# Kernel tuning notes

Hardware: AMD Instinct MI355X
Metric: run time of the kernel (lower is better)

## Reference

```python
import jax, jax.numpy as jnp
import numpy as np

WINDOW_SIZE = 11
SIGMA = 1.5
C1 = 0.01 ** 2
C2 = 0.03 ** 2


def _gaussian_window(window_size, sigma, channel):
    xs = np.arange(window_size)
    g = np.exp(-((xs - window_size // 2) ** 2) / (2.0 * sigma ** 2))
    g = (g / g.sum()).astype(np.float32)
    w2d = np.outer(g, g)  # [k,k]
    # depthwise kernel layout OIHW with O=channel, I=1
    return jnp.asarray(np.broadcast_to(w2d, (channel, 1, window_size, window_size)).copy())


def _blur(x, window, channel):
    # depthwise conv, SAME-style padding = k//2 (k odd -> exact SAME)
    pad = WINDOW_SIZE // 2
    return jax.lax.conv_general_dilated(
        x, window,
        window_strides=(1, 1),
        padding=[(pad, pad), (pad, pad)],
        dimension_numbers=('NCHW', 'OIHW', 'NCHW'),
        feature_group_count=channel,
    )


def setup_inputs() -> dict:
    key = jax.random.key(0)
    k1, k2 = jax.random.split(key)
    shape = (32, 3, 512, 512)
    img1 = jax.random.uniform(k1, shape, dtype=jnp.float32)
    img2 = jax.random.uniform(k2, shape, dtype=jnp.float32)
    return {"img1": img1, "img2": img2}


def reference(img1, img2):
    channel = img1.shape[1]
    window = _gaussian_window(WINDOW_SIZE, SIGMA, channel).astype(img1.dtype)

    mu1 = _blur(img1, window, channel)
    mu2 = _blur(img2, window, channel)
    mu1_sq = mu1 * mu1
    mu2_sq = mu2 * mu2
    mu1_mu2 = mu1 * mu2

    sigma1_sq = _blur(img1 * img1, window, channel) - mu1_sq
    sigma2_sq = _blur(img2 * img2, window, channel) - mu2_sq
    sigma12 = _blur(img1 * img2, window, channel) - mu1_mu2

    ssim_map = ((2 * mu1_mu2 + C1) * (2 * sigma12 + C2)) / (
        (mu1_sq + mu2_sq + C1) * (sigma1_sq + sigma2_sq + C2))
    return 1.0 - jnp.mean(ssim_map)
```

## Files before the change

### kernel.cpp

```cpp
#include <hip/hip_runtime.h>


#define HH 512
#define WW 512
#define TILE 32
#define IN_ROWS 42
#define S_STRIDE 50
#define H_STRIDE 32
#define NPLANES 96
#define NPIX 25165824.0f
#define NACC 256
#define NTASK 672

#define H0123_OFF 0
#define H4_OFF  21504
#define UNION_BYTES 26880

typedef float v2f __attribute__((ext_vector_type(2)));
typedef float v4f __attribute__((ext_vector_type(4)));

__global__ __launch_bounds__(256, 6) void ssim_fused_kernel(
    const float* __restrict__ img1, const float* __restrict__ img2,
    float* __restrict__ acc) {
  __shared__ __align__(16) char ub[UNION_BYTES];
  __shared__ float wsum[4];

  v2f (*s12)[S_STRIDE] = (v2f (*)[S_STRIDE])ub;
  v4f (*h0123)[H_STRIDE] = (v4f (*)[H_STRIDE])(ub + H0123_OFF);
  float (*h4)[H_STRIDE] = (float (*)[H_STRIDE])(ub + H4_OFF);

  const int tid = threadIdx.x;
  const int tx = blockIdx.x * TILE;
  const int ty = blockIdx.y * TILE;
  const size_t base = (size_t)blockIdx.z * (HH * WW);

  const float g[11] = {
      1.0283800e-03f, 7.5987600e-03f, 3.6000770e-02f, 1.0936072e-01f,
      2.1300560e-01f, 2.6601170e-01f, 2.1300560e-01f, 1.0936072e-01f,
      3.6000770e-02f, 7.5987600e-03f, 1.0283800e-03f};

#pragma unroll
  for (int it = 0; it < 2; ++it) {
    int idx = it * 256 + tid;
    if (idx < IN_ROWS * 12) {
      int r = idx / 12;
      int p = idx - r * 12;
      int gy = ty - 5 + r;
      int gx = tx - 8 + 4 * p;
      v4f A = {0.f, 0.f, 0.f, 0.f}, B = {0.f, 0.f, 0.f, 0.f};
      if ((unsigned)gy < (unsigned)HH && (unsigned)gx < (unsigned)WW) {
        size_t off = base + (size_t)gy * WW + gx;
        A = *(const v4f*)(img1 + off);
        B = *(const v4f*)(img2 + off);
      }
      *(v4f*)&s12[r][4 * p]     = (v4f){A.x, B.x, A.y, B.y};
      *(v4f*)&s12[r][4 * p + 2] = (v4f){A.z, B.z, A.w, B.w};
    }
  }
  __syncthreads();

  v2f hold01[3][2], hold23[3][2], hold4[3];
#pragma unroll
  for (int t = 0; t < 3; ++t) {
    int idx = t * 256 + tid;
    if (idx < NTASK) {
      int r = idx >> 4;
      int c = (idx & 15) * 2;
      const v4f* qp = (const v4f*)&s12[r][c + 2];
      v4f q0 = qp[0], q1 = qp[1], q2 = qp[2], q3 = qp[3];
      v4f q4 = qp[4], q5 = qp[5], q6 = qp[6];
      v2f P[14];
      P[0]  = (v2f){q0.x, q0.y};  P[1]  = (v2f){q0.z, q0.w};
      P[2]  = (v2f){q1.x, q1.y};  P[3]  = (v2f){q1.z, q1.w};
      P[4]  = (v2f){q2.x, q2.y};  P[5]  = (v2f){q2.z, q2.w};
      P[6]  = (v2f){q3.x, q3.y};  P[7]  = (v2f){q3.z, q3.w};
      P[8]  = (v2f){q4.x, q4.y};  P[9]  = (v2f){q4.z, q4.w};
      P[10] = (v2f){q5.x, q5.y};  P[11] = (v2f){q5.z, q5.w};
      P[12] = (v2f){q6.x, q6.y};  P[13] = (v2f){q6.z, q6.w};

      v2f a01_0 = (v2f){0.f, 0.f}, a23_0 = (v2f){0.f, 0.f};
      v2f a01_1 = (v2f){0.f, 0.f}, a23_1 = (v2f){0.f, 0.f};
      float a4_0 = 0.f, a4_1 = 0.f;
#pragma unroll
      for (int k = 1; k <= 12; ++k) {
        v2f p = P[k];
        v2f sq = p * p;
        float cr = p.x * p.y;
        if (k <= 11) {
          float w = g[k - 1];
          a01_0 += w * p;
          a23_0 += w * sq;
          a4_0 = __builtin_fmaf(w, cr, a4_0);
        }
        if (k >= 2) {
          float w = g[k - 2];
          a01_1 += w * p;
          a23_1 += w * sq;
          a4_1 = __builtin_fmaf(w, cr, a4_1);
        }
      }
      hold01[t][0] = a01_0;  hold01[t][1] = a01_1;
      hold23[t][0] = a23_0;  hold23[t][1] = a23_1;
      hold4[t] = (v2f){a4_0, a4_1};
    }
  }
  __syncthreads();

#pragma unroll
  for (int t = 0; t < 3; ++t) {
    int idx = t * 256 + tid;
    if (idx < NTASK) {
      int r = idx >> 4;
      int c = (idx & 15) * 2;
      *(v4f*)&h0123[r][c]     = (v4f){hold01[t][0].x, hold01[t][0].y,
                                      hold23[t][0].x, hold23[t][0].y};
      *(v4f*)&h0123[r][c + 1] = (v4f){hold01[t][1].x, hold01[t][1].y,
                                      hold23[t][1].x, hold23[t][1].y};
      *(v2f*)&h4[r][c] = hold4[t];
    }
  }
  __syncthreads();

  const float C1 = 1e-4f;
  const float C2 = 9e-4f;
  const int c = tid & 31;
  const int r0 = (tid >> 5) * 4;

  v2f m[4], vv[4];
  float b12[4];
#pragma unroll
  for (int o = 0; o < 4; ++o) {
    m[o] = (v2f){0.f, 0.f};
    vv[o] = (v2f){0.f, 0.f};
    b12[o] = 0.f;
  }

#pragma unroll
  for (int dy = 0; dy < 14; ++dy) {
    v4f q = h0123[r0 + dy][c];
    v2f a = (v2f){q.x, q.y};
    v2f b = (v2f){q.z, q.w};
    float d = h4[r0 + dy][c];
#pragma unroll
    for (int o = 0; o < 4; ++o) {
      const int k = dy - o;
      if (k >= 0 && k < 11) {
        float w = g[k];
        m[o] += w * a;
        vv[o] += w * b;
        b12[o] = __builtin_fmaf(w, d, b12[o]);
      }
    }
  }

  float lsum = 0.f;
#pragma unroll
  for (int o = 0; o < 4; ++o) {
    float mu1 = m[o].x, mu2 = m[o].y;
    float mu1sq = mu1 * mu1;
    float mu2sq = mu2 * mu2;
    float mu12 = mu1 * mu2;
    float sig11 = vv[o].x - mu1sq;
    float sig22 = vv[o].y - mu2sq;
    float sig12 = b12[o] - mu12;
    float num = (2.f * mu12 + C1) * (2.f * sig12 + C2);
    float den = (mu1sq + mu2sq + C1) * (sig11 + sig22 + C2);
    lsum += num * __builtin_amdgcn_rcpf(den);
  }

#pragma unroll
  for (int off = 32; off > 0; off >>= 1)
    lsum += __shfl_down(lsum, off, 64);
  const int lane = tid & 63;
  const int wid = tid >> 6;
  if (lane == 0) wsum[wid] = lsum;
  __syncthreads();
  if (tid == 0) {
    float b = wsum[0] + wsum[1] + wsum[2] + wsum[3];
    int slot = (blockIdx.x + blockIdx.y * 16 + blockIdx.z) & (NACC - 1);
    atomicAdd(acc + slot, b);
  }
}

__global__ void ssim_finalize_kernel(const float* __restrict__ acc,
                                     float* __restrict__ out) {
  __shared__ float wsum[4];
  const int tid = threadIdx.x;
  float s = acc[tid];
#pragma unroll
  for (int off = 32; off > 0; off >>= 1)
    s += __shfl_down(s, off, 64);
  if ((tid & 63) == 0) wsum[tid >> 6] = s;
  __syncthreads();
  if (tid == 0)
    out[0] = 1.0f - (wsum[0] + wsum[1] + wsum[2] + wsum[3]) * (1.0f / NPIX);
}

extern "C" void kernel_launch(void* const* d_in, const int* in_sizes, int n_in,
                              void* d_out, int out_size, void* d_ws, size_t ws_size,
                              hipStream_t stream) {
  const float* img1 = (const float*)d_in[0];
  const float* img2 = (const float*)d_in[1];
  float* out = (float*)d_out;
  float* acc = (float*)d_ws;

  (void)hipMemsetAsync(acc, 0, NACC * sizeof(float), stream);

  dim3 grid(WW / TILE, HH / TILE, NPLANES);
  ssim_fused_kernel<<<grid, 256, 0, stream>>>(img1, img2, acc);
  ssim_finalize_kernel<<<1, NACC, 0, stream>>>(acc, out);
}
```

Baseline: 279.7 us.

## Use 32x64 tiles with 4-wide horizontal and 8-row vertical register blocking

```diff
diff --git a/kernel.cpp b/kernel.cpp
--- a/kernel.cpp
+++ b/kernel.cpp
@@ -3,35 +3,37 @@
 
 #define HH 512
 #define WW 512
-#define TILE 32
-#define IN_ROWS 42
+#define TW 32
+#define TH 64
+#define IN_ROWS 74
 #define S_STRIDE 50
-#define H_STRIDE 32
+#define HSTRIDE 32
 #define NPLANES 96
 #define NPIX 25165824.0f
 #define NACC 256
-#define NTASK 672
+#define NT1 888
+#define NT2 592
 
 #define H0123_OFF 0
-#define H4_OFF  21504
-#define UNION_BYTES 26880
+#define H4_OFF 37888
+#define UNION_BYTES 47360
 
 typedef float v2f __attribute__((ext_vector_type(2)));
 typedef float v4f __attribute__((ext_vector_type(4)));
 
-__global__ __launch_bounds__(256, 6) void ssim_fused_kernel(
+__global__ __launch_bounds__(256, 3) void ssim_fused_kernel(
     const float* __restrict__ img1, const float* __restrict__ img2,
     float* __restrict__ acc) {
   __shared__ __align__(16) char ub[UNION_BYTES];
   __shared__ float wsum[4];
 
   v2f (*s12)[S_STRIDE] = (v2f (*)[S_STRIDE])ub;
-  v4f (*h0123)[H_STRIDE] = (v4f (*)[H_STRIDE])(ub + H0123_OFF);
-  float (*h4)[H_STRIDE] = (float (*)[H_STRIDE])(ub + H4_OFF);
+  v4f (*h0123)[HSTRIDE] = (v4f (*)[HSTRIDE])(ub + H0123_OFF);
+  float (*h4)[HSTRIDE] = (float (*)[HSTRIDE])(ub + H4_OFF);
 
   const int tid = threadIdx.x;
-  const int tx = blockIdx.x * TILE;
-  const int ty = blockIdx.y * TILE;
+  const int tx = blockIdx.x * TW;
+  const int ty = blockIdx.y * TH;
   const size_t base = (size_t)blockIdx.z * (HH * WW);
 
   const float g[11] = {
@@ -40,9 +42,9 @@
       3.6000770e-02f, 7.5987600e-03f, 1.0283800e-03f};
 
 #pragma unroll
-  for (int it = 0; it < 2; ++it) {
+  for (int it = 0; it < 4; ++it) {
     int idx = it * 256 + tid;
-    if (idx < IN_ROWS * 12) {
+    if (idx < NT1) {
       int r = idx / 12;
       int p = idx - r * 12;
       int gy = ty - 5 + r;
@@ -59,49 +61,70 @@
   }
   __syncthreads();
 
-  v2f hold01[3][2], hold23[3][2], hold4[3];
+  v2f h01h[3][4], h23h[3][4], h4h[3][2];
 #pragma unroll
   for (int t = 0; t < 3; ++t) {
     int idx = t * 256 + tid;
-    if (idx < NTASK) {
-      int r = idx >> 4;
-      int c = (idx & 15) * 2;
+    if (idx < NT2) {
+      int r = idx >> 3;
+      int cq = idx & 7;
+      int c = cq << 2;
       const v4f* qp = (const v4f*)&s12[r][c + 2];
-      v4f q0 = qp[0], q1 = qp[1], q2 = qp[2], q3 = qp[3];
-      v4f q4 = qp[4], q5 = qp[5], q6 = qp[6];
-      v2f P[14];
-      P[0]  = (v2f){q0.x, q0.y};  P[1]  = (v2f){q0.z, q0.w};
-      P[2]  = (v2f){q1.x, q1.y};  P[3]  = (v2f){q1.z, q1.w};
-      P[4]  = (v2f){q2.x, q2.y};  P[5]  = (v2f){q2.z, q2.w};
-      P[6]  = (v2f){q3.x, q3.y};  P[7]  = (v2f){q3.z, q3.w};
-      P[8]  = (v2f){q4.x, q4.y};  P[9]  = (v2f){q4.z, q4.w};
-      P[10] = (v2f){q5.x, q5.y};  P[11] = (v2f){q5.z, q5.w};
-      P[12] = (v2f){q6.x, q6.y};  P[13] = (v2f){q6.z, q6.w};
-
-      v2f a01_0 = (v2f){0.f, 0.f}, a23_0 = (v2f){0.f, 0.f};
-      v2f a01_1 = (v2f){0.f, 0.f}, a23_1 = (v2f){0.f, 0.f};
-      float a4_0 = 0.f, a4_1 = 0.f;
-#pragma unroll
-      for (int k = 1; k <= 12; ++k) {
-        v2f p = P[k];
+      v4f q[8];
+#pragma unroll
+      for (int m = 0; m < 8; ++m) q[m] = qp[m];
+      v2f P[16];
+#pragma unroll
+      for (int m = 0; m < 8; ++m) {
+        P[2 * m]     = (v2f){q[m].x, q[m].y};
+        P[2 * m + 1] = (v2f){q[m].z, q[m].w};
+      }
+
+      v2f a01[4], a23[4], a4p[2];
+#pragma unroll
+      for (int j = 0; j < 4; ++j) {
+        a01[j] = (v2f){0.f, 0.f};
+        a23[j] = (v2f){0.f, 0.f};
+      }
+      a4p[0] = (v2f){0.f, 0.f};
+      a4p[1] = (v2f){0.f, 0.f};
+
+#pragma unroll
+      for (int i = 0; i < 16; ++i) {
+        v2f p = P[i];
         v2f sq = p * p;
         float cr = p.x * p.y;
-        if (k <= 11) {
-          float w = g[k - 1];
-          a01_0 += w * p;
-          a23_0 += w * sq;
-          a4_0 = __builtin_fmaf(w, cr, a4_0);
+#pragma unroll
+        for (int j = 0; j < 4; ++j) {
+          int k = i - 1 - j;
+          if (k >= 0 && k <= 10) {
+            float w = g[k];
+            a01[j] += w * p;
+            a23[j] += w * sq;
+          }
         }
-        if (k >= 2) {
-          float w = g[k - 2];
-          a01_1 += w * p;
-          a23_1 += w * sq;
-          a4_1 = __builtin_fmaf(w, cr, a4_1);
+        {
+          int k0 = i - 1, k1 = i - 2;
+          bool u0 = (k0 >= 0 && k0 <= 10), u1 = (k1 >= 0 && k1 <= 10);
+          if (u0 || u1) {
+            v2f w2 = (v2f){u0 ? g[k0] : 0.f, u1 ? g[k1] : 0.f};
+            a4p[0] += w2 * cr;
+          }
+          int k2 = i - 3, k3 = i - 4;
+          bool u2 = (k2 >= 0 && k2 <= 10), u3 = (k3 >= 0 && k3 <= 10);
+          if (u2 || u3) {
+            v2f w2 = (v2f){u2 ? g[k2] : 0.f, u3 ? g[k3] : 0.f};
+            a4p[1] += w2 * cr;
+          }
         }
       }
-      hold01[t][0] = a01_0;  hold01[t][1] = a01_1;
-      hold23[t][0] = a23_0;  hold23[t][1] = a23_1;
-      hold4[t] = (v2f){a4_0, a4_1};
+#pragma unroll
+      for (int j = 0; j < 4; ++j) {
+        h01h[t][j] = a01[j];
+        h23h[t][j] = a23[j];
+      }
+      h4h[t][0] = a4p[0];
+      h4h[t][1] = a4p[1];
     }
   }
   __syncthreads();
@@ -109,14 +132,19 @@
 #pragma unroll
   for (int t = 0; t < 3; ++t) {
     int idx = t * 256 + tid;
-    if (idx < NTASK) {
-      int r = idx >> 4;
-      int c = (idx & 15) * 2;
-      *(v4f*)&h0123[r][c]     = (v4f){hold01[t][0].x, hold01[t][0].y,
-                                      hold23[t][0].x, hold23[t][0].y};
-      *(v4f*)&h0123[r][c + 1] = (v4f){hold01[t][1].x, hold01[t][1].y,
-                                      hold23[t][1].x, hold23[t][1].y};
-      *(v2f*)&h4[r][c] = hold4[t];
+    if (idx < NT2) {
+      int r = idx >> 3;
+      int cq = idx & 7;
+      int rot = r & 7;
+#pragma unroll
+      for (int j = 0; j < 4; ++j) {
+        int pc = ((cq << 2) + j + rot) & 31;
+        h0123[r][pc] = (v4f){h01h[t][j].x, h01h[t][j].y,
+                             h23h[t][j].x, h23h[t][j].y};
+      }
+      int pg = (cq + rot) & 7;
+      *(v4f*)&h4[r][pg << 2] = (v4f){h4h[t][0].x, h4h[t][0].y,
+                                     h4h[t][1].x, h4h[t][1].y};
     }
   }
   __syncthreads();
@@ -124,45 +152,57 @@
   const float C1 = 1e-4f;
   const float C2 = 9e-4f;
   const int c = tid & 31;
-  const int r0 = (tid >> 5) * 4;
-
-  v2f m[4], vv[4];
-  float b12[4];
-#pragma unroll
-  for (int o = 0; o < 4; ++o) {
+  const int r0 = (tid >> 5) << 3;
+
+  v2f m[8], vv[8], b12p[4];
+#pragma unroll
+  for (int o = 0; o < 8; ++o) {
     m[o] = (v2f){0.f, 0.f};
     vv[o] = (v2f){0.f, 0.f};
-    b12[o] = 0.f;
-  }
-
-#pragma unroll
-  for (int dy = 0; dy < 14; ++dy) {
-    v4f q = h0123[r0 + dy][c];
+  }
+#pragma unroll
+  for (int pr = 0; pr < 4; ++pr) b12p[pr] = (v2f){0.f, 0.f};
+
+#pragma unroll
+  for (int dy = 0; dy < 18; ++dy) {
+    int rr = r0 + dy;
+    int rot = rr & 7;
+    int pc = (c + rot) & 31;
+    v4f q = h0123[rr][pc];
+    float d = h4[rr][((((c >> 2) + rot) & 7) << 2) + (c & 3)];
     v2f a = (v2f){q.x, q.y};
     v2f b = (v2f){q.z, q.w};
-    float d = h4[r0 + dy][c];
-#pragma unroll
-    for (int o = 0; o < 4; ++o) {
-      const int k = dy - o;
-      if (k >= 0 && k < 11) {
+#pragma unroll
+    for (int o = 0; o < 8; ++o) {
+      int k = dy - o;
+      if (k >= 0 && k <= 10) {
         float w = g[k];
         m[o] += w * a;
         vv[o] += w * b;
-        b12[o] = __builtin_fmaf(w, d, b12[o]);
+      }
+    }
+#pragma unroll
+    for (int pr = 0; pr < 4; ++pr) {
+      int k0 = dy - 2 * pr, k1 = k0 - 1;
+      bool u0 = (k0 >= 0 && k0 <= 10), u1 = (k1 >= 0 && k1 <= 10);
+      if (u0 || u1) {
+        v2f w2 = (v2f){u0 ? g[k0] : 0.f, u1 ? g[k1] : 0.f};
+        b12p[pr] += w2 * d;
       }
     }
   }
 
   float lsum = 0.f;
 #pragma unroll
-  for (int o = 0; o < 4; ++o) {
+  for (int o = 0; o < 8; ++o) {
     float mu1 = m[o].x, mu2 = m[o].y;
     float mu1sq = mu1 * mu1;
     float mu2sq = mu2 * mu2;
     float mu12 = mu1 * mu2;
+    float b12 = (o & 1) ? b12p[o >> 1].y : b12p[o >> 1].x;
     float sig11 = vv[o].x - mu1sq;
     float sig22 = vv[o].y - mu2sq;
-    float sig12 = b12[o] - mu12;
+    float sig12 = b12 - mu12;
     float num = (2.f * mu12 + C1) * (2.f * sig12 + C2);
     float den = (mu1sq + mu2sq + C1) * (sig11 + sig22 + C2);
     lsum += num * __builtin_amdgcn_rcpf(den);
@@ -206,7 +246,7 @@
 
   (void)hipMemsetAsync(acc, 0, NACC * sizeof(float), stream);
 
-  dim3 grid(WW / TILE, HH / TILE, NPLANES);
+  dim3 grid(WW / TW, HH / TH, NPLANES);
   ssim_fused_kernel<<<grid, 256, 0, stream>>>(img1, img2, acc);
   ssim_finalize_kernel<<<1, NACC, 0, stream>>>(acc, out);
 }
```

After: 308.7 us. +10.4%, slower.
